# Kernel tuning notes

Hardware: AMD Instinct MI355X
Metric: run time of the kernel (lower is better)

The kernel has to match this reference:

```python
import jax, jax.numpy as jnp
import numpy as np

B, T, CIN, H, W = 256, 19, 3, 24, 24
HID, LAST, K = 64, 128, 512
CC = 0.25  # commitment cost
NUM_DEC_LAYERS = 19


def setup_inputs() -> dict:
    key = jax.random.key(0)
    ks = jax.random.split(key, 19)
    def rn(k, shape, scale=0.05):
        return jax.random.normal(k, shape, jnp.float32) * scale
    return dict(
        x=jax.random.normal(ks[0], (B, T, CIN, H, W), jnp.float32),
        eps=jax.random.normal(ks[1], (B, LAST), jnp.float32),
        emb=jax.random.normal(ks[2], (K, HID), jnp.float32),
        enc_w0=rn(ks[3], (HID, CIN, 3, 3)), enc_w0_b=rn(ks[4], (HID,)),
        enc_w1=rn(ks[5], (2 * LAST, HID, 8, 8)), enc_w1_b=rn(ks[6], (2 * LAST,)),
        enc_r0=rn(ks[7], (HID, HID)), enc_r0_b=rn(ks[8], (HID,)),
        enc_lin_w=rn(ks[9], (2 * LAST, 2 * LAST)), enc_lin_b=rn(ks[10], (2 * LAST,)),
        dec_w0=rn(ks[11], (HID, CIN, 3, 3)), dec_w0_b=rn(ks[12], (CIN,)),
        dec_w1=rn(ks[13], (LAST, HID, 8, 8)), dec_w1_b=rn(ks[14], (HID,)),
        dec_r0=rn(ks[15], (HID, HID)), dec_r0_b=rn(ks[16], (HID,)),
        dec_lin_w=rn(ks[17], (LAST, LAST)), dec_lin_b=rn(ks[18], (LAST,)),
    )


def reference(x, eps, emb, enc_w0, enc_w0_b, enc_w1, enc_w1_b, enc_r0, enc_r0_b,
              enc_lin_w, enc_lin_b, dec_w0, dec_w0_b, dec_w1, dec_w1_b,
              dec_r0, dec_r0_b, dec_lin_w, dec_lin_b):
    relu = jax.nn.relu

    # ---- encoder (conv-RNN over time) ----
    def conv0(xt):  # Conv2d(CIN->HID, k=3, s=3): 24x24 -> 8x8
        y = jax.lax.conv_general_dilated(
            xt, enc_w0, (3, 3), 'VALID',
            dimension_numbers=('NCHW', 'OIHW', 'NCHW'))
        return y + enc_w0_b[None, :, None, None]

    def contract(h1):  # Conv2d(HID->2*LAST, k=8) on 8x8 == full contraction
        return jnp.einsum('bchw,ochw->bo', h1, enc_w1) + enc_w1_b

    h1 = relu(conv0(x[:, 0]))
    h2 = relu(contract(h1))

    def enc_step(carry, xt):
        h1, h2 = carry
        h1 = relu(conv0(xt) + jnp.einsum('bchw,oc->bohw', h1, enc_r0)
                  + enc_r0_b[None, :, None, None])
        h2h = relu(contract(h1))
        h2 = relu(h2h + h2 @ enc_lin_w.T + enc_lin_b)
        return (h1, h2), None

    (h1, h2), _ = jax.lax.scan(enc_step, (h1, h2), jnp.swapaxes(x[:, 1:], 0, 1))

    # ---- VQ (EMA codebook lookup; codebook carries no grad) ----
    zin = jnp.transpose(h1, (0, 2, 3, 1))        # [B, 8, 8, HID]
    flat = zin.reshape(-1, HID)                   # [B*64, HID]
    d = (jnp.sum(flat * flat, 1, keepdims=True)
         + jnp.sum(emb * emb, 1) - 2.0 * flat @ emb.T)
    idx = jnp.argmin(d, 1)                        # [B*64]
    q = emb[idx].reshape(zin.shape)
    loss_vq = CC * jnp.mean((jax.lax.stop_gradient(q) - zin) ** 2)
    q_st = zin + jax.lax.stop_gradient(q - zin)   # straight-through
    quantized = jnp.transpose(q_st, (0, 3, 1, 2)) # [B, HID, 8, 8]
    counts = jnp.zeros((K,), flat.dtype).at[idx].add(1.0)
    avg = counts / flat.shape[0]
    perplexity = jnp.exp(-jnp.sum(avg * jnp.log(avg + 1e-10)))

    # ---- KL(q(z|x) || N(0,1)) and reparam sample ----
    mu, logvar = jnp.split(h2, 2, axis=1)
    kl = jnp.mean(jnp.sum(0.5 * (jnp.exp(logvar) + mu * mu - 1.0 - logvar), axis=1))
    h2s = mu + jnp.exp(0.5 * logvar) * eps

    # ---- decoder (conv-RNN emitting 19 frames) ----
    def dec_update(h1c, h2c):
        h2c = relu(h2c @ dec_lin_w.T + dec_lin_b)
        h1h = jnp.einsum('bchw,oc->bohw', h1c, dec_r0) + dec_r0_b[None, :, None, None]
        h1l = jnp.einsum('bc,cohw->bohw', h2c, dec_w1) + dec_w1_b[None, :, None, None]
        return relu(h1h + h1l), h2c

    h1d, h2d = dec_update(quantized, h2s)  # i == 0: no emitted frame

    def dec_step(carry, _):
        h1c, h2c = carry
        h1c, h2c = dec_update(h1c, h2c)
        # ConvTranspose2d(HID->CIN, k=3, s=3): non-overlapping -> einsum + reshape
        y = jnp.einsum('bchw,coij->bohiwj', h1c, dec_w0).reshape(
            h1c.shape[0], CIN, 24, 24)
        layer = jax.nn.elu(y + dec_w0_b[None, :, None, None])
        return (h1c, h2c), layer

    _, layers = jax.lax.scan(dec_step, (h1d, h2d), None, length=NUM_DEC_LAYERS)
    x_tilde = jnp.swapaxes(layers, 0, 1)  # [B, 19, CIN, 24, 24]

    return (loss_vq, kl, x_tilde, perplexity)
```

## Files before the change

kernel.cpp:

```cpp
#include <hip/hip_runtime.h>
#include <math.h>

#define RL(x) __builtin_amdgcn_readfirstlane(x)

typedef short  s16x8 __attribute__((ext_vector_type(8)));
typedef float  f32x4 __attribute__((ext_vector_type(4)));

__device__ __forceinline__ float relu_(float v) { return v > 0.f ? v : 0.f; }
__device__ __forceinline__ unsigned short f2bf(float f) {
  unsigned u = __float_as_uint(f);
  u += 0x7FFFu + ((u >> 16) & 1u);
  return (unsigned short)(u >> 16);
}
__device__ __forceinline__ float bf2f(unsigned short h) {
  return __uint_as_float((unsigned)h << 16);
}

__global__ __launch_bounds__(256) void k_prep(
    const float* __restrict__ w1, const float* __restrict__ linw,
    const float* __restrict__ dlinw, const float* __restrict__ emb,
    const float* __restrict__ dw1,
    unsigned short* __restrict__ w1b, float* __restrict__ linT,
    float* __restrict__ dlinT, float* __restrict__ embsq,
    unsigned short* __restrict__ dw1b,
    float* __restrict__ scal, float* __restrict__ counts)
{
  int bid = blockIdx.x, tid = threadIdx.x;
  if (bid < 64) {
    #pragma unroll
    for (int j = 0; j < 32; ++j) {
      int idx = bid * 16384 + j * 512 + tid * 2;
      float2 v = *(const float2*)(w1 + idx);
      unsigned pk = ((unsigned)f2bf(v.y) << 16) | (unsigned)f2bf(v.x);
      *(unsigned*)&w1b[idx] = pk;
    }
    return;
  }
  if (bid == 84) {
    if (tid < 2) scal[tid] = 0.f;
    for (int j = tid; j < 512; j += 256) counts[j] = 0.f;
    return;
  }
  if (bid >= 85) {
    __shared__ float tbuf[64 * 65];
    int idx = bid - 85;
    int r0 = (idx >> 6) * 64, c0 = (idx & 63) * 64;
    int lane = tid & 63, grp = tid >> 6;
    for (int pp = 0; pp < 16; ++pp) {
      int rr = pp * 4 + grp;
      tbuf[rr * 65 + lane] = dw1[(size_t)(r0 + rr) * 4096 + c0 + lane];
    }
    __syncthreads();
    for (int pp = 0; pp < 16; ++pp) {
      int cc = pp * 4 + grp;
      dw1b[(size_t)(c0 + cc) * 128 + r0 + lane] = f2bf(tbuf[lane * 65 + cc]);
    }
    return;
  }
  if (bid >= 82) {
    int k = (bid - 82) * 256 + tid;
    const float* e = emb + k * 64;
    float s0 = 0, s1 = 0, s2 = 0, s3 = 0;
    #pragma unroll
    for (int c = 0; c < 64; c += 4) {
      s0 += e[c] * e[c]; s1 += e[c+1] * e[c+1];
      s2 += e[c+2] * e[c+2]; s3 += e[c+3] * e[c+3];
    }
    embsq[k] = (s0 + s1) + (s2 + s3);
    return;
  }
  __shared__ float buf[64 * 65];
  const float* in; float* out; int R, C, tr, tc;
  if (bid < 80) { in = linw;  out = linT;  R = 256; C = 256; tr = (bid - 64) >> 2; tc = (bid - 64) & 3; }
  else          { in = dlinw; out = dlinT; R = 128; C = 128; tr = (bid - 80) >> 1; tc = (bid - 80) & 1; }
  int r0 = tr * 64, c0 = tc * 64;
  int lane = tid & 63, grp = tid >> 6;
  for (int pp = 0; pp < 16; ++pp) {
    int rr = pp * 4 + grp;
    buf[rr * 65 + lane] = in[(r0 + rr) * C + c0 + lane];
  }
  __syncthreads();
  for (int pp = 0; pp < 16; ++pp) {
    int cc = pp * 4 + grp;
    out[(c0 + cc) * R + r0 + lane] = buf[lane * 65 + cc];
  }
}

__device__ __forceinline__ void loadx27(const float* __restrict__ xb,
                                        float* xv) {
  #pragma unroll
  for (int c = 0; c < 3; ++c)
    #pragma unroll
    for (int ki = 0; ki < 3; ++ki) {
      const float* r = xb + c * 576 + ki * 24;
      float2 v01 = *(const float2*)r;
      float  v2  = r[2];
      xv[c * 9 + ki * 3 + 0] = v01.x;
      xv[c * 9 + ki * 3 + 1] = v01.y;
      xv[c * 9 + ki * 3 + 2] = v2;
    }
}
__device__ __forceinline__ void prod8(const float* __restrict__ wb,
                                      const float* xv, float* cvrow, int l) {
  #pragma unroll
  for (int q = 0; q < 8; ++q) {
    const float* wr = wb + q * 27;
    float c0 = 0, c1 = 0, c2 = 0;
    #pragma unroll
    for (int m = 0; m < 27; m += 3) {
      c0 += xv[m] * wr[m]; c1 += xv[m+1] * wr[m+1]; c2 += xv[m+2] * wr[m+2];
    }
    cvrow[q * 64 + l] = (c0 + c1) + c2;
  }
}

__global__ __launch_bounds__(1024) void k_encmma(
    const float* __restrict__ x,
    const float* __restrict__ w0, const float* __restrict__ w0b,
    const float* __restrict__ r0, const float* __restrict__ r0b,
    unsigned short* __restrict__ st_out,
    unsigned short* __restrict__ st_tail,
    float* __restrict__ h1f)
{
  __shared__ unsigned short Hs[2][4096];
  __shared__ float CV[2][4096];
  int b = blockIdx.x, tid = threadIdx.x;
  int l = tid & 63;
  int wv = RL(tid >> 6);

  if (wv >= 8) {
    int pw = wv - 8;
    int ip = l >> 3, jp = l & 7;
    const float* xbase = x + ((size_t)b * 19 * 3) * 576 + (ip * 3) * 24 + jp * 3;
    const float* wb = w0 + pw * 8 * 27;
    float* cvrow0 = &CV[0][pw * 8 * 64];
    float* cvrow1 = &CV[1][pw * 8 * 64];

    float xv[27];
    loadx27(xbase, xv);
    prod8(wb, xv, cvrow0, l);
    loadx27(xbase + (size_t)3 * 576, xv);
    __syncthreads();

    for (int t = 0; t <= 18; ++t) {
      if (t < 18) {
        prod8(wb, xv, (((t + 1) & 1) ? cvrow1 : cvrow0), l);
        if (t < 17)
          loadx27(xbase + (size_t)(t + 2) * 3 * 576, xv);
      }
      __syncthreads();
    }
    return;
  }

  int os = wv >> 1, ph = wv & 1;
  int co = os * 16 + (l >> 4) * 4;
  int arow = os * 16 + (l & 15);
  s16x8 avR[2];
  #pragma unroll
  for (int kk = 0; kk < 2; ++kk) {
    int cb = (kk * 4 + (l >> 4)) * 8;
    const float* src = r0 + arow * 64 + cb;
    #pragma unroll
    for (int j = 0; j < 8; ++j) avR[kk][j] = (short)f2bf(src[j]);
  }
  float b0v[4], b1v[4];
  #pragma unroll
  for (int r = 0; r < 4; ++r) {
    b0v[r] = w0b[co + r];
    b1v[r] = b0v[r] + r0b[co + r];
  }
  int pA = ph * 32 + (l & 15);
  int pB = pA + 16;
  __syncthreads();

  for (int t = 0; t <= 18; ++t) {
    f32x4 accA = (f32x4){0.f, 0.f, 0.f, 0.f};
    f32x4 accB = (f32x4){0.f, 0.f, 0.f, 0.f};
    if (t > 0) {
      const unsigned short* cbuf = Hs[(t & 1) ^ 1];
      #pragma unroll
      for (int kk = 0; kk < 2; ++kk) {
        int chk = kk * 4 + (l >> 4);
        s16x8 bvA = *(const s16x8*)&cbuf[pA * 64 + ((chk ^ (pA & 7)) << 3)];
        s16x8 bvB = *(const s16x8*)&cbuf[pB * 64 + ((chk ^ (pB & 7)) << 3)];
        accA = __builtin_amdgcn_mfma_f32_16x16x32_bf16(avR[kk], bvA, accA, 0, 0, 0);
        accB = __builtin_amdgcn_mfma_f32_16x16x32_bf16(avR[kk], bvB, accB, 0, 0, 0);
      }
    }
    const float* cv = CV[t & 1];
    unsigned short* so = (t < 16)
        ? st_out  + (size_t)t * 1048576 + (size_t)b * 4096
        : st_tail + (size_t)(t - 16) * 1048576 + (size_t)b * 4096;
    unsigned short* nb = Hs[t & 1];
    {
      float v0 = relu_(accA[0] + cv[(co + 0) * 64 + pA] + (t ? b1v[0] : b0v[0]));
      float v1 = relu_(accA[1] + cv[(co + 1) * 64 + pA] + (t ? b1v[1] : b0v[1]));
      float v2 = relu_(accA[2] + cv[(co + 2) * 64 + pA] + (t ? b1v[2] : b0v[2]));
      float v3 = relu_(accA[3] + cv[(co + 3) * 64 + pA] + (t ? b1v[3] : b0v[3]));
      uint2 pk;
      pk.x = (unsigned)f2bf(v0) | ((unsigned)f2bf(v1) << 16);
      pk.y = (unsigned)f2bf(v2) | ((unsigned)f2bf(v3) << 16);
      *(uint2*)&nb[pA * 64 + (((co >> 3) ^ (pA & 7)) << 3) + (co & 7)] = pk;
      so[(co + 0) * 64 + pA] = (unsigned short)(pk.x & 0xFFFF);
      so[(co + 1) * 64 + pA] = (unsigned short)(pk.x >> 16);
      so[(co + 2) * 64 + pA] = (unsigned short)(pk.y & 0xFFFF);
      so[(co + 3) * 64 + pA] = (unsigned short)(pk.y >> 16);
      if (t == 18) {
        h1f[(size_t)b * 4096 + (co + 0) * 64 + pA] = v0;
        h1f[(size_t)b * 4096 + (co + 1) * 64 + pA] = v1;
        h1f[(size_t)b * 4096 + (co + 2) * 64 + pA] = v2;
        h1f[(size_t)b * 4096 + (co + 3) * 64 + pA] = v3;
      }
    }
    {
      float v0 = relu_(accB[0] + cv[(co + 0) * 64 + pB] + (t ? b1v[0] : b0v[0]));
      float v1 = relu_(accB[1] + cv[(co + 1) * 64 + pB] + (t ? b1v[1] : b0v[1]));
      float v2 = relu_(accB[2] + cv[(co + 2) * 64 + pB] + (t ? b1v[2] : b0v[2]));
      float v3 = relu_(accB[3] + cv[(co + 3) * 64 + pB] + (t ? b1v[3] : b0v[3]));
      uint2 pk;
      pk.x = (unsigned)f2bf(v0) | ((unsigned)f2bf(v1) << 16);
      pk.y = (unsigned)f2bf(v2) | ((unsigned)f2bf(v3) << 16);
      *(uint2*)&nb[pB * 64 + (((co >> 3) ^ (pB & 7)) << 3) + (co & 7)] = pk;
      so[(co + 0) * 64 + pB] = (unsigned short)(pk.x & 0xFFFF);
      so[(co + 1) * 64 + pB] = (unsigned short)(pk.x >> 16);
      so[(co + 2) * 64 + pB] = (unsigned short)(pk.y & 0xFFFF);
      so[(co + 3) * 64 + pB] = (unsigned short)(pk.y >> 16);
      if (t == 18) {
        h1f[(size_t)b * 4096 + (co + 0) * 64 + pB] = v0;
        h1f[(size_t)b * 4096 + (co + 1) * 64 + pB] = v1;
        h1f[(size_t)b * 4096 + (co + 2) * 64 + pB] = v2;
        h1f[(size_t)b * 4096 + (co + 3) * 64 + pB] = v3;
      }
    }
    __syncthreads();
  }
}

__global__ __launch_bounds__(256) void k_conmma8(
    const unsigned short* __restrict__ st_out,
    const unsigned short* __restrict__ st_tail,
    const unsigned short* __restrict__ w1b,
    float* __restrict__ partsk)
{
  __shared__ unsigned short As[32 * 64];
  __shared__ unsigned short Bs[128 * 64];
  int bid = blockIdx.x, tid = threadIdx.x;
  int kts = bid & 7;
  int rem0 = bid >> 3;
  int t = rem0 >> 4, rem = rem0 & 15;
  int mt = rem >> 1, nt = rem & 1;
  int b0 = mt * 32, n0 = nt * 128;
  const unsigned short* abase = ((t < 16)
      ? st_out  + (size_t)t * 1048576
      : st_tail + (size_t)(t - 16) * 1048576) + (size_t)b0 * 4096;
  int w = RL(tid >> 6), l = tid & 63;
  int rh = w >> 1, chf = w & 1;

  int ar = tid >> 3, ac = tid & 7;
  unsigned short* adst = &As[ar * 64 + ((ac ^ (ar & 7)) << 3)];
  const unsigned short* asrc = abase + (size_t)ar * 4096 + (ac << 3);

  f32x4 acc[4];
  #pragma unroll
  for (int u = 0; u < 4; ++u) acc[u] = (f32x4){0.f, 0.f, 0.f, 0.f};

  for (int kt = 0; kt < 8; ++kt) {
    int k0 = kts * 512 + kt * 64;
    __syncthreads();
    *(s16x8*)adst = *(const s16x8*)(asrc + k0);
    #pragma unroll
    for (int cc = 0; cc < 4; ++cc) {
      int idx = cc * 256 + tid;
      int br = idx >> 3, bc = idx & 7;
      *(s16x8*)&Bs[br * 64 + ((bc ^ (br & 7)) << 3)] =
          *(const s16x8*)(w1b + (size_t)(n0 + br) * 4096 + k0 + (bc << 3));
    }
    __syncthreads();
    #pragma unroll
    for (int kk = 0; kk < 2; ++kk) {
      int arw = rh * 16 + (l & 15);
      int chk = kk * 4 + (l >> 4);
      s16x8 av = *(const s16x8*)&As[arw * 64 + ((chk ^ (arw & 7)) << 3)];
      #pragma unroll
      for (int u = 0; u < 4; ++u) {
        int brow = (chf * 4 + u) * 16 + (l & 15);
        s16x8 bv = *(const s16x8*)&Bs[brow * 64 + ((chk ^ (brow & 7)) << 3)];
        acc[u] = __builtin_amdgcn_mfma_f32_16x16x32_bf16(av, bv, acc[u], 0, 0, 0);
      }
    }
  }
  float* pb = partsk + (size_t)kts * 1245184 + (size_t)t * 65536;
  int colbase = n0 + chf * 64 + (l & 15);
  int rowbase = b0 + rh * 16 + (l >> 4) * 4;
  #pragma unroll
  for (int u = 0; u < 4; ++u)
    #pragma unroll
    for (int r = 0; r < 4; ++r)
      pb[(size_t)(rowbase + r) * 256 + colbase + u * 16] = acc[u][r];
}

__global__ __launch_bounds__(256) void k_conmma(
    const unsigned short* __restrict__ st_out,
    const unsigned short* __restrict__ st_tail,
    const unsigned short* __restrict__ w1b,
    float* __restrict__ parts)
{
  __shared__ unsigned short As[32 * 64];
  __shared__ unsigned short Bs[128 * 64];
  int bid = blockIdx.x, tid = threadIdx.x;
  int t = bid >> 4, rem = bid & 15;
  int mt = rem >> 1, nt = rem & 1;
  int b0 = mt * 32, n0 = nt * 128;
  const unsigned short* abase = ((t < 16)
      ? st_out  + (size_t)t * 1048576
      : st_tail + (size_t)(t - 16) * 1048576) + (size_t)b0 * 4096;
  int w = RL(tid >> 6), l = tid & 63;
  int rh = w >> 1, chf = w & 1;

  int ar = tid >> 3, ac = tid & 7;
  unsigned short* adst = &As[ar * 64 + ((ac ^ (ar & 7)) << 3)];
  const unsigned short* asrc = abase + (size_t)ar * 4096 + (ac << 3);

  f32x4 acc[4];
  #pragma unroll
  for (int u = 0; u < 4; ++u) acc[u] = (f32x4){0.f, 0.f, 0.f, 0.f};

  for (int kt = 0; kt < 64; ++kt) {
    int k0 = kt * 64;
    __syncthreads();
    *(s16x8*)adst = *(const s16x8*)(asrc + k0);
    #pragma unroll
    for (int cc = 0; cc < 4; ++cc) {
      int idx = cc * 256 + tid;
      int br = idx >> 3, bc = idx & 7;
      *(s16x8*)&Bs[br * 64 + ((bc ^ (br & 7)) << 3)] =
          *(const s16x8*)(w1b + (size_t)(n0 + br) * 4096 + k0 + (bc << 3));
    }
    __syncthreads();
    #pragma unroll
    for (int kk = 0; kk < 2; ++kk) {
      int arw = rh * 16 + (l & 15);
      int chk = kk * 4 + (l >> 4);
      s16x8 av = *(const s16x8*)&As[arw * 64 + ((chk ^ (arw & 7)) << 3)];
      #pragma unroll
      for (int u = 0; u < 4; ++u) {
        int brow = (chf * 4 + u) * 16 + (l & 15);
        s16x8 bv = *(const s16x8*)&Bs[brow * 64 + ((chk ^ (brow & 7)) << 3)];
        acc[u] = __builtin_amdgcn_mfma_f32_16x16x32_bf16(av, bv, acc[u], 0, 0, 0);
      }
    }
  }
  float* pb = parts + (size_t)t * 65536;
  int colbase = n0 + chf * 64 + (l & 15);
  int rowbase = b0 + rh * 16 + (l >> 4) * 4;
  #pragma unroll
  for (int u = 0; u < 4; ++u)
    #pragma unroll
    for (int r = 0; r < 4; ++r)
      pb[(size_t)(rowbase + r) * 256 + colbase + u * 16] = acc[u][r];
}

__global__ __launch_bounds__(512, 1) void k_h2all(
    const float* __restrict__ partsk, int nslc,
    const float* __restrict__ w1b,
    const float* __restrict__ linT, const float* __restrict__ linb,
    const float* __restrict__ eps, float* __restrict__ scal,
    const float* __restrict__ dlinT, const float* __restrict__ dlinb,
    unsigned short* __restrict__ h2b)
{
  __shared__ float partsL[4864];
  __shared__ float curL[256];
  __shared__ float ppart[512];
  __shared__ float red[256];
  int b = blockIdx.x, tid = threadIdx.x;
  const size_t SL = 1245184;
  for (int idx = tid; idx < 4864; idx += 512) {
    size_t off = (size_t)(idx >> 8) * 65536 + (size_t)b * 256 + (idx & 255);
    if (nslc == 8) {
      float s0 = partsk[off]          + partsk[SL + off];
      float s1 = partsk[2 * SL + off] + partsk[3 * SL + off];
      float s2 = partsk[4 * SL + off] + partsk[5 * SL + off];
      float s3 = partsk[6 * SL + off] + partsk[7 * SL + off];
      partsL[idx] = (s0 + s1) + (s2 + s3);
    } else {
      partsL[idx] = partsk[off];
    }
  }
  int o  = tid & 255, kh = tid >> 8;
  float wreg[128];
  #pragma unroll
  for (int jj = 0; jj < 128; ++jj)
    wreg[jj] = linT[(kh * 128 + jj) * 256 + o];
  __syncthreads();

  if (tid < 256)
    curL[tid] = relu_(partsL[tid] + w1b[tid]);
  __syncthreads();
  for (int t = 1; t <= 18; ++t) {
    float lacc = 0.f;
    #pragma unroll
    for (int jj = 0; jj < 128; ++jj)
      lacc += wreg[jj] * curL[kh * 128 + jj];
    ppart[tid] = lacc;
    __syncthreads();
    if (tid < 256) {
      float h2h = relu_(partsL[t * 256 + tid] + w1b[tid]);
      curL[tid] = relu_(h2h + ppart[tid] + ppart[256 + tid] + linb[tid]);
    }
    __syncthreads();
  }
  if (tid < 128) {
    float mu = curL[tid], lv = curL[128 + tid];
    red[tid] = 0.5f * (expf(lv) + mu * mu - 1.0f - lv);
  }
  __syncthreads();
  for (int s = 64; s > 0; s >>= 1) {
    if (tid < s) red[tid] += red[tid + s];
    __syncthreads();
  }
  if (tid == 0) atomicAdd(&scal[1], red[0]);
  float hs = 0.f;
  if (tid < 128)
    hs = curL[tid] + expf(0.5f * curL[128 + tid]) * eps[(size_t)b * 128 + tid];
  __syncthreads();
  if (tid < 128) curL[tid] = hs;
  __syncthreads();

  int o2 = tid & 127, kh2 = (tid >> 7) & 1;
  float wreg2[64];
  if (tid < 256) {
    #pragma unroll
    for (int jj = 0; jj < 64; ++jj)
      wreg2[jj] = dlinT[(kh2 * 64 + jj) * 128 + o2];
  }
  for (int s = 0; s < 20; ++s) {
    if (tid < 256) {
      float lacc = 0.f;
      #pragma unroll
      for (int jj = 0; jj < 64; ++jj)
        lacc += wreg2[jj] * curL[kh2 * 64 + jj];
      ppart[tid] = lacc;
    }
    __syncthreads();
    if (tid < 128) {
      float v = relu_(ppart[tid] + ppart[128 + tid] + dlinb[tid]);
      h2b[(size_t)s * 32768 + (size_t)b * 128 + tid] = f2bf(v);
      curL[tid] = v;
    }
    __syncthreads();
  }
}

__global__ __launch_bounds__(256) void k_argmin(
    const float* __restrict__ h1f, const float* __restrict__ emb,
    const float* __restrict__ embsq,
    float* __restrict__ pbest, int* __restrict__ pidx)
{
  __shared__ float sd[256];
  __shared__ int   sk[256];
  int bid = blockIdx.x, tid = threadIdx.x;
  int qtr = bid >> 8, b = bid & 255;
  int p = tid & 63, kg = RL(tid >> 6);
  float f[64];
  const float* hb = h1f + (size_t)b * 4096 + p;
  #pragma unroll
  for (int c = 0; c < 64; ++c) f[c] = hb[c * 64];
  float best = 3.4e38f; int bk = 0;
  int kbeg = qtr * 128 + kg * 32;
  for (int k = kbeg; k < kbeg + 32; ++k) {
    const float* er = emb + k * 64;
    float d0 = 0, d1 = 0, d2 = 0, d3 = 0;
    #pragma unroll
    for (int c = 0; c < 64; c += 4) {
      d0 += f[c] * er[c];     d1 += f[c+1] * er[c+1];
      d2 += f[c+2] * er[c+2]; d3 += f[c+3] * er[c+3];
    }
    float d = embsq[k] - 2.f * ((d0 + d1) + (d2 + d3));
    if (d < best) { best = d; bk = k; }
  }
  sd[tid] = best; sk[tid] = bk;
  __syncthreads();
  if (tid < 64) {
    float bb = sd[tid]; int kk = sk[tid];
    #pragma unroll
    for (int g = 1; g < 4; ++g) {
      float dg = sd[g * 64 + tid];
      if (dg < bb) { bb = dg; kk = sk[g * 64 + tid]; }
    }
    pbest[qtr * 16384 + b * 64 + tid] = bb;
    pidx [qtr * 16384 + b * 64 + tid] = kk;
  }
}

__device__ __forceinline__ unsigned short* h1l_ptr(
    int d, int b, float* out, unsigned short* tail)
{
  if (d >= 1 && d <= 17)
    return (unsigned short*)(out + 2 + (size_t)b * 32832 + (size_t)(d - 1) * 1728);
  int slot = (d == 0) ? 0 : (d - 17);
  return tail + (size_t)slot * 1048576 + (size_t)b * 4096;
}

__global__ __launch_bounds__(256) void k_declmma(
    const unsigned short* __restrict__ h2b,
    const unsigned short* __restrict__ dw1b,
    float* __restrict__ out, unsigned short* __restrict__ tail)
{
  __shared__ unsigned short As[64 * 128];
  __shared__ unsigned short Bs[64 * 128];
  int bid = blockIdx.x, tid = threadIdx.x;
  int mt = bid >> 6, nt = bid & 63;
  int m0 = mt * 64, n0 = nt * 64;
  int w = RL(tid >> 6), l = tid & 63;

  #pragma unroll
  for (int cc = 0; cc < 4; ++cc) {
    int idx = cc * 256 + tid;
    int row = idx >> 4, col = idx & 15;
    *(s16x8*)&As[row * 128 + ((col ^ (row & 7)) << 3)] =
        *(const s16x8*)(h2b + (size_t)(m0 + row) * 128 + (col << 3));
    *(s16x8*)&Bs[row * 128 + ((col ^ (row & 7)) << 3)] =
        *(const s16x8*)(dw1b + (size_t)(n0 + row) * 128 + (col << 3));
  }
  __syncthreads();

  f32x4 acc[4];
  #pragma unroll
  for (int u = 0; u < 4; ++u) acc[u] = (f32x4){0.f, 0.f, 0.f, 0.f};
  int arow = w * 16 + (l & 15);
  #pragma unroll
  for (int kk = 0; kk < 4; ++kk) {
    int chk = kk * 4 + (l >> 4);
    s16x8 av = *(const s16x8*)&As[arow * 128 + ((chk ^ (arow & 7)) << 3)];
    #pragma unroll
    for (int u = 0; u < 4; ++u) {
      int brow = u * 16 + (l & 15);
      s16x8 bv = *(const s16x8*)&Bs[brow * 128 + ((chk ^ (brow & 7)) << 3)];
      acc[u] = __builtin_amdgcn_mfma_f32_16x16x32_bf16(av, bv, acc[u], 0, 0, 0);
    }
  }
  int d = m0 >> 8;
  #pragma unroll
  for (int r = 0; r < 4; ++r) {
    int b = (m0 & 255) + w * 16 + (l >> 4) * 4 + r;
    unsigned short* op = h1l_ptr(d, b, out, tail);
    #pragma unroll
    for (int u = 0; u < 4; ++u)
      op[n0 + u * 16 + (l & 15)] = f2bf(acc[u][r]);
  }
}

__global__ __launch_bounds__(256) void k_vqstats(
    const float* __restrict__ h1f, const float* __restrict__ emb,
    const float* __restrict__ pbest, const int* __restrict__ pidx,
    float* __restrict__ Q, float* __restrict__ counts,
    float* __restrict__ loss_sum)
{
  __shared__ int   fk[64];
  __shared__ int   lhist[512];
  __shared__ float red[256];
  int b = blockIdx.x, tid = threadIdx.x;
  for (int j = tid; j < 512; j += 256) lhist[j] = 0;
  __syncthreads();
  if (tid < 64) {
    float bb = pbest[b * 64 + tid];
    int   kk = pidx [b * 64 + tid];
    #pragma unroll
    for (int q = 1; q < 4; ++q) {
      float dq = pbest[q * 16384 + b * 64 + tid];
      if (dq < bb) { bb = dq; kk = pidx[q * 16384 + b * 64 + tid]; }
    }
    fk[tid] = kk;
    atomicAdd(&lhist[kk], 1);
  }
  __syncthreads();
  int p = tid & 63, cgi = tid >> 6;
  int kk = fk[p];
  const float* eb = emb + kk * 64 + cgi * 16;
  const float* hz = h1f + (size_t)b * 4096 + cgi * 1024 + p;
  float* qb = Q + (size_t)b * 4096 + cgi * 1024 + p;
  float ls = 0;
  #pragma unroll
  for (int c = 0; c < 16; ++c) {
    float e = eb[c];
    float z = hz[c * 64];
    float dd = e - z;
    ls += dd * dd;
    qb[c * 64] = e;
  }
  red[tid] = ls;
  __syncthreads();
  for (int s = 128; s > 0; s >>= 1) { if (tid < s) red[tid] += red[tid + s]; __syncthreads(); }
  if (tid == 0) atomicAdd(loss_sum, red[0]);
  for (int j = tid; j < 512; j += 256) {
    int h = lhist[j];
    if (h > 0) atomicAdd(&counts[j], (float)h);
  }
}

__global__ __launch_bounds__(1024) void k_decchain(
    const float* __restrict__ Q,
    const float* __restrict__ dr0, const float* __restrict__ dr0b,
    const float* __restrict__ dw1b_bias,
    const float* __restrict__ w0d, const float* __restrict__ w0db,
    float* __restrict__ out, unsigned short* __restrict__ tail,
    const float* __restrict__ counts, const float* __restrict__ scal)
{
  int bid = blockIdx.x, tid = threadIdx.x;
  if (bid == 256) {
    __shared__ float red[512];
    if (tid < 512) {
      float avg = counts[tid] * (1.0f / 16384.0f);
      red[tid] = avg * logf(avg + 1e-10f);
    }
    __syncthreads();
    for (int s = 256; s > 0; s >>= 1) {
      if (tid < s) red[tid] += red[tid + s];
      __syncthreads();
    }
    if (tid == 0) {
      out[0] = 0.25f * scal[0] * (1.0f / 1048576.0f);
      out[1] = scal[1] * (1.0f / 256.0f);
      out[2 + 8404992] = expf(-red[0]);
    }
    return;
  }
  __shared__ unsigned short Hs[2][4096];
  int b = bid;
  int l = tid & 63;
  int wv = RL(tid >> 6);

  for (int idx = tid; idx < 4096; idx += 1024) {
    int c = idx >> 6, p = idx & 63;
    Hs[0][p * 64 + ((((c >> 3) ^ (p & 7))) << 3) + (c & 7)] =
        f2bf(Q[(size_t)b * 4096 + idx]);
  }

  if (wv < 8) {
    int os = wv >> 1;
    int ph = wv & 1;
    int co = os * 16 + (l >> 4) * 4;
    int arow = os * 16 + (l & 15);
    s16x8 avR[2];
    #pragma unroll
    for (int kk = 0; kk < 2; ++kk) {
      int cb = (kk * 4 + (l >> 4)) * 8;
      const float* src = dr0 + arow * 64 + cb;
      #pragma unroll
      for (int j = 0; j < 8; ++j) avR[kk][j] = (short)f2bf(src[j]);
    }
    float biasv[4];
    #pragma unroll
    for (int r = 0; r < 4; ++r) biasv[r] = dr0b[co + r] + dw1b_bias[co + r];
    int pA = (ph * 2) * 16 + (l & 15);
    int pB = (ph * 2 + 1) * 16 + (l & 15);
    __syncthreads();

    for (int i = 0; i <= 20; ++i) {
      if (i <= 19) {
        const unsigned short* lp = h1l_ptr(i, b, out, tail);
        float hlA[4], hlB[4];
        #pragma unroll
        for (int r = 0; r < 4; ++r) {
          hlA[r] = bf2f(lp[(co + r) * 64 + pA]);
          hlB[r] = bf2f(lp[(co + r) * 64 + pB]);
        }
        const unsigned short* cb = Hs[i & 1];
        f32x4 accA = (f32x4){0.f, 0.f, 0.f, 0.f};
        f32x4 accB = (f32x4){0.f, 0.f, 0.f, 0.f};
        #pragma unroll
        for (int kk = 0; kk < 2; ++kk) {
          int chk = kk * 4 + (l >> 4);
          s16x8 bvA = *(const s16x8*)&cb[pA * 64 + ((chk ^ (pA & 7)) << 3)];
          s16x8 bvB = *(const s16x8*)&cb[pB * 64 + ((chk ^ (pB & 7)) << 3)];
          accA = __builtin_amdgcn_mfma_f32_16x16x32_bf16(avR[kk], bvA, accA, 0, 0, 0);
          accB = __builtin_amdgcn_mfma_f32_16x16x32_bf16(avR[kk], bvB, accB, 0, 0, 0);
        }
        unsigned short* nb = Hs[(i + 1) & 1];
        {
          float v0 = relu_(accA[0] + hlA[0] + biasv[0]);
          float v1 = relu_(accA[1] + hlA[1] + biasv[1]);
          float v2 = relu_(accA[2] + hlA[2] + biasv[2]);
          float v3 = relu_(accA[3] + hlA[3] + biasv[3]);
          uint2 pk;
          pk.x = (unsigned)f2bf(v0) | ((unsigned)f2bf(v1) << 16);
          pk.y = (unsigned)f2bf(v2) | ((unsigned)f2bf(v3) << 16);
          *(uint2*)&nb[pA * 64 + (((co >> 3) ^ (pA & 7)) << 3) + (co & 7)] = pk;
        }
        {
          float v0 = relu_(accB[0] + hlB[0] + biasv[0]);
          float v1 = relu_(accB[1] + hlB[1] + biasv[1]);
          float v2 = relu_(accB[2] + hlB[2] + biasv[2]);
          float v3 = relu_(accB[3] + hlB[3] + biasv[3]);
          uint2 pk;
          pk.x = (unsigned)f2bf(v0) | ((unsigned)f2bf(v1) << 16);
          pk.y = (unsigned)f2bf(v2) | ((unsigned)f2bf(v3) << 16);
          *(uint2*)&nb[pB * 64 + (((co >> 3) ^ (pB & 7)) << 3) + (co & 7)] = pk;
        }
      }
      __syncthreads();
    }
  } else {
    int job = wv - 8;
    int mt = job >> 2, pt = job & 3;
    int m0 = mt * 16 + (l >> 4) * 4;
    int am = mt * 16 + (l & 15);
    s16x8 avE[2];
    #pragma unroll
    for (int kk = 0; kk < 2; ++kk) {
      int cbg = (kk * 4 + (l >> 4)) * 8;
      #pragma unroll
      for (int j = 0; j < 8; ++j)
        avE[kk][j] = (am < 27) ? (short)f2bf(w0d[(cbg + j) * 27 + am]) : (short)0;
    }
    int p = pt * 16 + (l & 15);
    int hrow = p >> 3, wcol = p & 7;
    int preoff[4]; float eb[4]; bool vld[4];
    #pragma unroll
    for (int r = 0; r < 4; ++r) {
      int m = m0 + r;
      vld[r] = (m < 27);
      int mm = vld[r] ? m : 0;
      int o3 = mm / 9, rr = mm % 9, ki = rr / 3, kj = rr % 3;
      preoff[r] = o3 * 576 + (hrow * 3 + ki) * 24 + wcol * 3 + kj;
      eb[r] = w0db[o3];
    }
    __syncthreads();

    for (int i = 0; i <= 20; ++i) {
      if (i >= 2) {
        const unsigned short* cb = Hs[i & 1];
        f32x4 acc = (f32x4){0.f, 0.f, 0.f, 0.f};
        #pragma unroll
        for (int kk = 0; kk < 2; ++kk) {
          int chk = kk * 4 + (l >> 4);
          s16x8 bv = *(const s16x8*)&cb[p * 64 + ((chk ^ (p & 7)) << 3)];
          acc = __builtin_amdgcn_mfma_f32_16x16x32_bf16(avE[kk], bv, acc, 0, 0, 0);
        }
        int t = i - 2;
        float* fb = out + 2 + (size_t)(b * 19 + t) * 1728;
        #pragma unroll
        for (int r = 0; r < 4; ++r) {
          if (vld[r]) {
            float v = acc[r] + eb[r];
            v = v > 0.f ? v : expm1f(v);
            fb[preoff[r]] = v;
          }
        }
      }
      __syncthreads();
    }
  }
}

extern "C" void kernel_launch(void* const* d_in, const int* in_sizes, int n_in,
                              void* d_out, int out_size, void* d_ws, size_t ws_size,
                              hipStream_t stream)
{
  const float* x     = (const float*)d_in[0];
  const float* eps   = (const float*)d_in[1];
  const float* emb   = (const float*)d_in[2];
  const float* ew0   = (const float*)d_in[3];
  const float* ew0b  = (const float*)d_in[4];
  const float* ew1   = (const float*)d_in[5];
  const float* ew1b  = (const float*)d_in[6];
  const float* er0   = (const float*)d_in[7];
  const float* er0b  = (const float*)d_in[8];
  const float* elinw = (const float*)d_in[9];
  const float* elinb = (const float*)d_in[10];
  const float* dw0   = (const float*)d_in[11];
  const float* dw0b  = (const float*)d_in[12];
  const float* dw1   = (const float*)d_in[13];
  const float* dw1b  = (const float*)d_in[14];
  const float* dr0   = (const float*)d_in[15];
  const float* dr0b  = (const float*)d_in[16];
  const float* dlinw = (const float*)d_in[17];
  const float* dlinb = (const float*)d_in[18];
  float* out = (float*)d_out;
  float* ws  = (float*)d_ws;

  unsigned short* W1B = (unsigned short*)ws;
  float* Q      = ws + 0;
  float* LINT   = ws + 1048576;
  float* DLINT  = ws + 1114112;
  float* EMBSQ  = ws + 1130496;
  float* H1F    = ws + 1131008;
  float* PARTS  = ws + 2179584;
  float* PBEST  = ws + 2179584;
  int*   PIDX   = (int*)(ws + 2245120);
  unsigned short* TAIL = (unsigned short*)(ws + 3424768);
  unsigned short* H2B  = (unsigned short*)(ws + 4997632);
  unsigned short* DW1B = (unsigned short*)(ws + 5325312);
  float* SCAL   = ws + 5652992;
  float* COUNTS = ws + 5652994;
  const size_t XC_OFF = 5653508;
  const size_t XC_END = XC_OFF + (size_t)8 * 1245184;
  bool big = ws_size >= XC_END * sizeof(float);
  float* PARTSK = big ? (ws + XC_OFF) : nullptr;

  unsigned short* ST_OUT = (unsigned short*)(out + 2);

  k_prep<<<213, 256, 0, stream>>>(ew1, elinw, dlinw, emb, dw1, W1B, LINT,
                                  DLINT, EMBSQ, DW1B, SCAL, COUNTS);
  k_encmma<<<256, 1024, 0, stream>>>(x, ew0, ew0b, er0, er0b,
                                     ST_OUT, TAIL, H1F);
  const float* parts_src;
  int nslc;
  if (big) {
    k_conmma8<<<2432, 256, 0, stream>>>(ST_OUT, TAIL, W1B, PARTSK);
    parts_src = PARTSK; nslc = 8;
  } else {
    k_conmma<<<304, 256, 0, stream>>>(ST_OUT, TAIL, W1B, PARTS);
    parts_src = PARTS; nslc = 1;
  }
  k_h2all<<<256, 512, 0, stream>>>(parts_src, nslc, ew1b, LINT, elinb, eps,
                                   SCAL, DLINT, dlinb, H2B);
  k_argmin<<<1024, 256, 0, stream>>>(H1F, emb, EMBSQ, PBEST, PIDX);
  k_declmma<<<5120, 256, 0, stream>>>(H2B, DW1B, out, TAIL);
  k_vqstats<<<256, 256, 0, stream>>>(H1F, emb, PBEST, PIDX, Q, COUNTS,
                                     &SCAL[0]);
  k_decchain<<<257, 1024, 0, stream>>>(Q, dr0, dr0b, dw1b, dw0, dw0b,
                                       out, TAIL, COUNTS, SCAL);
}
```

Before: 295.7 us.

## Merge conv0 producer warps into MFMA warps in encoder recurrence kernel

The encoder kernel previously split 16 waves into 8 MFMA waves (two 16-position tiles each) and 8 producer waves computing the 3x3 input conv for the next step. Now all 16 waves each handle one MFMA tile and also compute 4 conv0 output channels for the next timestep, so every wave does both roles. The CV shared buffer is padded to a row stride of 68 floats, apparently to reduce LDS bank conflicts on the transposed reads. This balances the work across waves and shortens the per-step critical path, at the cost of serialising conv work and MFMA work inside each wave.

Measured after the change: 308.4 us. 1.04x slower.

```diff
diff --git a/kernel.cpp b/kernel.cpp
--- a/kernel.cpp
+++ b/kernel.cpp
@@ -100,17 +100,17 @@
       xv[c * 9 + ki * 3 + 2] = v2;
     }
 }
-__device__ __forceinline__ void prod8(const float* __restrict__ wb,
-                                      const float* xv, float* cvrow, int l) {
-  #pragma unroll
-  for (int q = 0; q < 8; ++q) {
+__device__ __forceinline__ void prod4(const float* __restrict__ wb,
+                                      const float* xv, float* cvbase, int l) {
+  #pragma unroll
+  for (int q = 0; q < 4; ++q) {
     const float* wr = wb + q * 27;
     float c0 = 0, c1 = 0, c2 = 0;
     #pragma unroll
     for (int m = 0; m < 27; m += 3) {
       c0 += xv[m] * wr[m]; c1 += xv[m+1] * wr[m+1]; c2 += xv[m+2] * wr[m+2];
     }
-    cvrow[q * 64 + l] = (c0 + c1) + c2;
+    cvbase[q * 68 + l] = (c0 + c1) + c2;
   }
 }
 
@@ -123,37 +123,12 @@
     float* __restrict__ h1f)
 {
   __shared__ unsigned short Hs[2][4096];
-  __shared__ float CV[2][4096];
+  __shared__ float CV[2][4352];
   int b = blockIdx.x, tid = threadIdx.x;
   int l = tid & 63;
   int wv = RL(tid >> 6);
 
-  if (wv >= 8) {
-    int pw = wv - 8;
-    int ip = l >> 3, jp = l & 7;
-    const float* xbase = x + ((size_t)b * 19 * 3) * 576 + (ip * 3) * 24 + jp * 3;
-    const float* wb = w0 + pw * 8 * 27;
-    float* cvrow0 = &CV[0][pw * 8 * 64];
-    float* cvrow1 = &CV[1][pw * 8 * 64];
-
-    float xv[27];
-    loadx27(xbase, xv);
-    prod8(wb, xv, cvrow0, l);
-    loadx27(xbase + (size_t)3 * 576, xv);
-    __syncthreads();
-
-    for (int t = 0; t <= 18; ++t) {
-      if (t < 18) {
-        prod8(wb, xv, (((t + 1) & 1) ? cvrow1 : cvrow0), l);
-        if (t < 17)
-          loadx27(xbase + (size_t)(t + 2) * 3 * 576, xv);
-      }
-      __syncthreads();
-    }
-    return;
-  }
-
-  int os = wv >> 1, ph = wv & 1;
+  int os = wv >> 2, pq = wv & 3;
   int co = os * 16 + (l >> 4) * 4;
   int arow = os * 16 + (l & 15);
   s16x8 avR[2];
@@ -170,22 +145,29 @@
     b0v[r] = w0b[co + r];
     b1v[r] = b0v[r] + r0b[co + r];
   }
-  int pA = ph * 32 + (l & 15);
-  int pB = pA + 16;
+  int p = pq * 16 + (l & 15);
+
+  int ip = l >> 3, jp = l & 7;
+  const float* xbase = x + ((size_t)b * 19 * 3) * 576 + (ip * 3) * 24 + jp * 3;
+  const float* wb = w0 + wv * 4 * 27;
+  float* cvrow0 = &CV[0][wv * 4 * 68];
+  float* cvrow1 = &CV[1][wv * 4 * 68];
+
+  float xv[27];
+  loadx27(xbase, xv);
+  prod4(wb, xv, cvrow0, l);
+  loadx27(xbase + (size_t)3 * 576, xv);
   __syncthreads();
 
   for (int t = 0; t <= 18; ++t) {
-    f32x4 accA = (f32x4){0.f, 0.f, 0.f, 0.f};
-    f32x4 accB = (f32x4){0.f, 0.f, 0.f, 0.f};
+    f32x4 acc = (f32x4){0.f, 0.f, 0.f, 0.f};
     if (t > 0) {
       const unsigned short* cbuf = Hs[(t & 1) ^ 1];
       #pragma unroll
       for (int kk = 0; kk < 2; ++kk) {
         int chk = kk * 4 + (l >> 4);
-        s16x8 bvA = *(const s16x8*)&cbuf[pA * 64 + ((chk ^ (pA & 7)) << 3)];
-        s16x8 bvB = *(const s16x8*)&cbuf[pB * 64 + ((chk ^ (pB & 7)) << 3)];
-        accA = __builtin_amdgcn_mfma_f32_16x16x32_bf16(avR[kk], bvA, accA, 0, 0, 0);
-        accB = __builtin_amdgcn_mfma_f32_16x16x32_bf16(avR[kk], bvB, accB, 0, 0, 0);
+        s16x8 bv = *(const s16x8*)&cbuf[p * 64 + ((chk ^ (p & 7)) << 3)];
+        acc = __builtin_amdgcn_mfma_f32_16x16x32_bf16(avR[kk], bv, acc, 0, 0, 0);
       }
     }
     const float* cv = CV[t & 1];
@@ -194,44 +176,29 @@
         : st_tail + (size_t)(t - 16) * 1048576 + (size_t)b * 4096;
     unsigned short* nb = Hs[t & 1];
     {
-      float v0 = relu_(accA[0] + cv[(co + 0) * 64 + pA] + (t ? b1v[0] : b0v[0]));
-      float v1 = relu_(accA[1] + cv[(co + 1) * 64 + pA] + (t ? b1v[1] : b0v[1]));
-      float v2 = relu_(accA[2] + cv[(co + 2) * 64 + pA] + (t ? b1v[2] : b0v[2]));
-      float v3 = relu_(accA[3] + cv[(co + 3) * 64 + pA] + (t ? b1v[3] : b0v[3]));
+      float v0 = relu_(acc[0] + cv[(co + 0) * 68 + p] + (t ? b1v[0] : b0v[0]));
+      float v1 = relu_(acc[1] + cv[(co + 1) * 68 + p] + (t ? b1v[1] : b0v[1]));
+      float v2 = relu_(acc[2] + cv[(co + 2) * 68 + p] + (t ? b1v[2] : b0v[2]));
+      float v3 = relu_(acc[3] + cv[(co + 3) * 68 + p] + (t ? b1v[3] : b0v[3]));
       uint2 pk;
       pk.x = (unsigned)f2bf(v0) | ((unsigned)f2bf(v1) << 16);
       pk.y = (unsigned)f2bf(v2) | ((unsigned)f2bf(v3) << 16);
-      *(uint2*)&nb[pA * 64 + (((co >> 3) ^ (pA & 7)) << 3) + (co & 7)] = pk;
-      so[(co + 0) * 64 + pA] = (unsigned short)(pk.x & 0xFFFF);
-      so[(co + 1) * 64 + pA] = (unsigned short)(pk.x >> 16);
-      so[(co + 2) * 64 + pA] = (unsigned short)(pk.y & 0xFFFF);
-      so[(co + 3) * 64 + pA] = (unsigned short)(pk.y >> 16);
+      *(uint2*)&nb[p * 64 + (((co >> 3) ^ (p & 7)) << 3) + (co & 7)] = pk;
+      so[(co + 0) * 64 + p] = (unsigned short)(pk.x & 0xFFFF);
+      so[(co + 1) * 64 + p] = (unsigned short)(pk.x >> 16);
+      so[(co + 2) * 64 + p] = (unsigned short)(pk.y & 0xFFFF);
+      so[(co + 3) * 64 + p] = (unsigned short)(pk.y >> 16);
       if (t == 18) {
-        h1f[(size_t)b * 4096 + (co + 0) * 64 + pA] = v0;
-        h1f[(size_t)b * 4096 + (co + 1) * 64 + pA] = v1;
-        h1f[(size_t)b * 4096 + (co + 2) * 64 + pA] = v2;
-        h1f[(size_t)b * 4096 + (co + 3) * 64 + pA] = v3;
+        h1f[(size_t)b * 4096 + (co + 0) * 64 + p] = v0;
+        h1f[(size_t)b * 4096 + (co + 1) * 64 + p] = v1;
+        h1f[(size_t)b * 4096 + (co + 2) * 64 + p] = v2;
+        h1f[(size_t)b * 4096 + (co + 3) * 64 + p] = v3;
       }
     }
-    {
-      float v0 = relu_(accB[0] + cv[(co + 0) * 64 + pB] + (t ? b1v[0] : b0v[0]));
-      float v1 = relu_(accB[1] + cv[(co + 1) * 64 + pB] + (t ? b1v[1] : b0v[1]));
-      float v2 = relu_(accB[2] + cv[(co + 2) * 64 + pB] + (t ? b1v[2] : b0v[2]));
-      float v3 = relu_(accB[3] + cv[(co + 3) * 64 + pB] + (t ? b1v[3] : b0v[3]));
-      uint2 pk;
-      pk.x = (unsigned)f2bf(v0) | ((unsigned)f2bf(v1) << 16);
-      pk.y = (unsigned)f2bf(v2) | ((unsigned)f2bf(v3) << 16);
-      *(uint2*)&nb[pB * 64 + (((co >> 3) ^ (pB & 7)) << 3) + (co & 7)] = pk;
-      so[(co + 0) * 64 + pB] = (unsigned short)(pk.x & 0xFFFF);
-      so[(co + 1) * 64 + pB] = (unsigned short)(pk.x >> 16);
-      so[(co + 2) * 64 + pB] = (unsigned short)(pk.y & 0xFFFF);
-      so[(co + 3) * 64 + pB] = (unsigned short)(pk.y >> 16);
-      if (t == 18) {
-        h1f[(size_t)b * 4096 + (co + 0) * 64 + pB] = v0;
-        h1f[(size_t)b * 4096 + (co + 1) * 64 + pB] = v1;
-        h1f[(size_t)b * 4096 + (co + 2) * 64 + pB] = v2;
-        h1f[(size_t)b * 4096 + (co + 3) * 64 + pB] = v3;
-      }
+    if (t < 18) {
+      prod4(wb, xv, (((t + 1) & 1) ? cvrow1 : cvrow0), l);
+      if (t < 17)
+        loadx27(xbase + (size_t)(t + 2) * 3 * 576, xv);
     }
     __syncthreads();
   }
```
